# Kernel optimization log

Hardware: AMD Instinct MI355X
Metric: run time of the kernel (lower is better)

Reference implementation:

```python
import jax, jax.numpy as jnp
import numpy as np

D = 1024        # model dim (== moe_inter_dim, required by Expert's x2*x3)
H = 1024        # expert hidden dim (moe_inter_dim)
E = 8           # n_routed_experts
K = 2           # n_activated_experts (top-k)
I = 2 * 1024    # shared-expert inter dim = n_shared_experts * moe_inter_dim
ROUTE_SCALE = 1.0


def setup_inputs() -> dict:
    key = jax.random.key(0)
    ks = jax.random.split(key, 12)
    s = lambda *sh: 1.0 / np.sqrt(sh[-1])
    return {
        "x":      jax.random.normal(ks[0], (1, 2048, D), jnp.float32),
        "gate_w": jax.random.normal(ks[1], (E, D), jnp.float32) * s(E, D),
        "w1":     jax.random.normal(ks[2], (E, H, D), jnp.float32) * s(H, D),
        "b1":     jax.random.normal(ks[3], (E, H), jnp.float32) * 0.01,
        "w2":     jax.random.normal(ks[4], (E, D, H), jnp.float32) * s(D, H),
        "b2":     jax.random.normal(ks[5], (E, D), jnp.float32) * 0.01,
        "w3":     jax.random.normal(ks[6], (E, H, D), jnp.float32) * s(H, D),
        "b3":     jax.random.normal(ks[7], (E, H), jnp.float32) * 0.01,
        "sw1":    jax.random.normal(ks[8], (I, D), jnp.float32) * s(I, D),
        "sw2":    jax.random.normal(ks[9], (I, D), jnp.float32) * s(I, D),
        "sw3":    jax.random.normal(ks[10], (D, I), jnp.float32) * s(D, I),
    }


def reference(x, gate_w, w1, b1, w2, b2, w3, b3, sw1, sw2, sw3):
    B, S, _ = x.shape
    xt = x.reshape(-1, D)                                  # (T, D)
    # ---- Gate (softmax scoring, n_groups==1, no bias, route_scale=1) ----
    logits = xt @ gate_w.T                                 # (T, E)
    scores = jax.nn.softmax(logits.astype(jnp.float32), axis=-1)
    top_vals, idx = jax.lax.top_k(scores, K)               # (T, K)
    weights = (jnp.take_along_axis(scores, idx, axis=1)
               .astype(x.dtype)) * ROUTE_SCALE             # (T, K)
    # ---- Routed experts: input is scaled by routing weight BEFORE expert ----
    xs = xt[:, None, :] * weights[:, :, None]              # (T, K, D)
    y = jnp.zeros_like(xt)
    for e in range(E):  # fixed small loop over experts (dense masked dispatch)
        mask = (idx == e).astype(x.dtype)                  # (T, K)
        h = jax.nn.silu(jnp.einsum('tkd,hd->tkh', xs, w1[e]) + b1[e])
        x2 = jnp.einsum('tkh,dh->tkd', h, w2[e]) + b2[e]   # (T, K, D)
        x3 = jnp.einsum('tkd,hd->tkh', xs, w3[e]) + b3[e]  # (T, K, H==D)
        y = y + jnp.sum((x2 * x3) * mask[:, :, None], axis=1)
    # ---- Shared experts (SwiGLU MLP, no biases) ----
    z = (jax.nn.silu(xt @ sw1.T) * (xt @ sw2.T)) @ sw3.T   # (T, D)
    return (y + z).reshape(B, S, D)
```

## Files before the change

kernel.cpp:

```cpp
#include <hip/hip_runtime.h>

typedef unsigned short u16;
typedef __attribute__((ext_vector_type(4))) float floatx4;
typedef __attribute__((ext_vector_type(8))) short short8;

#define MAXROWS 5120

__device__ __forceinline__ u16 f2bf(float f) {
    union { float f; unsigned u; } v; v.f = f;
    unsigned r = v.u + 0x7FFF + ((v.u >> 16) & 1);
    return (u16)(r >> 16);
}
__device__ __forceinline__ float bf2f(u16 h) {
    union { unsigned u; float f; } v; v.u = ((unsigned)h) << 16; return v.f;
}
__device__ __forceinline__ float silu_f(float x) { return x / (1.f + __expf(-x)); }

__device__ __forceinline__ void gl_lds16(const void* g, void* l) {
    __builtin_amdgcn_global_load_lds(
        (__attribute__((address_space(1))) unsigned int*)g,
        (__attribute__((address_space(3))) unsigned int*)l, 16, 0, 0);
}

__device__ __forceinline__ void ld_frags(
    unsigned a0, unsigned a1, unsigned a2, unsigned a3,
    unsigned b0, unsigned b1, unsigned b2, unsigned b3,
    short8& af0, short8& af1, short8& af2, short8& af3,
    short8& bf0, short8& bf1, short8& bf2, short8& bf3) {
    asm volatile(
        "ds_read_b128 %0, %8\n\t"
        "ds_read_b128 %1, %9\n\t"
        "ds_read_b128 %2, %10\n\t"
        "ds_read_b128 %3, %11\n\t"
        "ds_read_b128 %4, %12\n\t"
        "ds_read_b128 %5, %13\n\t"
        "ds_read_b128 %6, %14\n\t"
        "ds_read_b128 %7, %15\n\t"
        "s_waitcnt lgkmcnt(0)"
        : "=&v"(af0), "=&v"(af1), "=&v"(af2), "=&v"(af3),
          "=&v"(bf0), "=&v"(bf1), "=&v"(bf2), "=&v"(bf3)
        : "v"(a0), "v"(a1), "v"(a2), "v"(a3),
          "v"(b0), "v"(b1), "v"(b2), "v"(b3));
}

#define WAIT_VM6() __builtin_amdgcn_s_waitcnt(3958)
#define WAIT_VM3() __builtin_amdgcn_s_waitcnt(3955)
#define WAIT_VM0() __builtin_amdgcn_s_waitcnt(3952)
#define BAR()      __builtin_amdgcn_s_barrier()

__global__ void conv_gate(const float* __restrict__ w1, const float* __restrict__ w2,
                          const float* __restrict__ w3, const float* __restrict__ sw1,
                          const float* __restrict__ sw2, const float* __restrict__ sw3,
                          const float* __restrict__ x, const float* __restrict__ gw,
                          u16* __restrict__ W13, u16* __restrict__ W2b,
                          u16* __restrict__ S12, u16* __restrict__ S3b,
                          u16* __restrict__ Xb,
                          int* __restrict__ idxA, float* __restrict__ wA) {
    int bid = blockIdx.x;
    if (bid < 512) {
        int w = threadIdx.x >> 6, lane = threadIdx.x & 63;
        int t = bid * 4 + w;
        const float* xr = x + (size_t)t * 1024;
        float acc[8];
#pragma unroll
        for (int e = 0; e < 8; e++) acc[e] = 0.f;
#pragma unroll
        for (int i = 0; i < 16; i++) {
            float xv = xr[lane + (i << 6)];
#pragma unroll
            for (int e = 0; e < 8; e++) acc[e] += xv * gw[e * 1024 + lane + (i << 6)];
        }
#pragma unroll
        for (int e = 0; e < 8; e++)
            for (int off = 32; off > 0; off >>= 1) acc[e] += __shfl_xor(acc[e], off);
        if (lane == 0) {
            float m = acc[0];
#pragma unroll
            for (int e = 1; e < 8; e++) m = fmaxf(m, acc[e]);
            float p[8], s = 0.f;
#pragma unroll
            for (int e = 0; e < 8; e++) { p[e] = __expf(acc[e] - m); s += p[e]; }
            float inv = 1.f / s;
#pragma unroll
            for (int e = 0; e < 8; e++) p[e] *= inv;
            int i0 = 0;
#pragma unroll
            for (int e = 1; e < 8; e++) if (p[e] > p[i0]) i0 = e;
            int i1 = (i0 == 0) ? 1 : 0;
            for (int e = i1 + 1; e < 8; e++) if (e != i0 && p[e] > p[i1]) i1 = e;
            idxA[2 * t] = i0; idxA[2 * t + 1] = i1;
            wA[2 * t] = p[i0]; wA[2 * t + 1] = p[i1];
        }
        return;
    }
    long j = (long)(bid - 512) * 256 + threadIdx.x;
    const float* src; u16* dst; long d;
    if (j < 2097152) {
        long e = j >> 18; src = w1; dst = W13; d = j + (e << 18);
    } else if ((j -= 2097152) < 2097152) {
        long e = j >> 18; src = w3; dst = W13; d = j + (e << 18) + 262144;
    } else if ((j -= 2097152) < 2097152) { src = w2;  dst = W2b; d = j; }
    else if ((j -= 2097152) < 524288) {
        long rr = j >> 8, c4 = j & 255;
        long br = ((rr >> 4) << 5) + (rr & 15);
        src = sw1; dst = S12; d = (br << 8) + c4;
    } else if ((j -= 524288) < 524288) {
        long rr = j >> 8, c4 = j & 255;
        long br = ((rr >> 4) << 5) + 16 + (rr & 15);
        src = sw2; dst = S12; d = (br << 8) + c4;
    } else if ((j -= 524288) < 524288)     { src = sw3; dst = S3b; d = j; }
    else { j -= 524288; src = x; dst = Xb; d = j; }
    float4 v = ((const float4*)src)[j];
    ushort4 o; o.x = f2bf(v.x); o.y = f2bf(v.y); o.z = f2bf(v.z); o.w = f2bf(v.w);
    ((ushort4*)dst)[d] = o;
}

__global__ void rank_k(const int* __restrict__ idxA, int* __restrict__ tileexp,
                       int* __restrict__ tilem0, int* __restrict__ tilevalid,
                       int* __restrict__ ntiles, int* __restrict__ slot_of) {
    int lane = threadIdx.x;
    const int4* my4 = (const int4*)(idxA + lane * 64);
    int h[8];
#pragma unroll
    for (int e = 0; e < 8; e++) h[e] = 0;
    for (int k = 0; k < 16; k++) {
        int4 t = my4[k];
#pragma unroll
        for (int e = 0; e < 8; e++)
            h[e] += (t.x == e) + (t.y == e) + (t.z == e) + (t.w == e);
    }
    int excl[8], tot[8];
#pragma unroll
    for (int e = 0; e < 8; e++) {
        int inc = h[e];
        for (int off = 1; off < 64; off <<= 1) {
            int up = __shfl_up(inc, off);
            if (lane >= off) inc += up;
        }
        excl[e] = inc - h[e];
        tot[e] = __shfl(inc, 63);
    }
    int base[8], tiles = 0;
#pragma unroll
    for (int e = 0; e < 8; e++) {
        base[e] = tiles * 128;
        tiles += (tot[e] + 127) >> 7;
    }
    if (lane == 0) {
        int t256 = 0;
        for (int e = 0; e < 8; e++) {
            int t128 = (tot[e] + 127) >> 7;
            for (int j = 0; j < t128; j += 2) {
                tileexp[t256] = e;
                tilem0[t256] = base[e] + (j << 7);
                tilevalid[t256] = ((t128 - j) >= 2) ? 256 : 128;
                t256++;
            }
        }
        ntiles[0] = t256;
    }
    int c[8];
#pragma unroll
    for (int e = 0; e < 8; e++) c[e] = base[e] + excl[e];
    int4* so4 = (int4*)(slot_of + lane * 64);
    for (int k = 0; k < 16; k++) {
        int4 t = my4[k];
        int4 s;
        int sx = 0;
#pragma unroll
        for (int e = 0; e < 8; e++) sx += (t.x == e) ? c[e] : 0;
#pragma unroll
        for (int e = 0; e < 8; e++) c[e] += (t.x == e);
        int sy = 0;
#pragma unroll
        for (int e = 0; e < 8; e++) sy += (t.y == e) ? c[e] : 0;
#pragma unroll
        for (int e = 0; e < 8; e++) c[e] += (t.y == e);
        int sz = 0;
#pragma unroll
        for (int e = 0; e < 8; e++) sz += (t.z == e) ? c[e] : 0;
#pragma unroll
        for (int e = 0; e < 8; e++) c[e] += (t.z == e);
        int sw = 0;
#pragma unroll
        for (int e = 0; e < 8; e++) sw += (t.w == e) ? c[e] : 0;
#pragma unroll
        for (int e = 0; e < 8; e++) c[e] += (t.w == e);
        s.x = sx; s.y = sy; s.z = sz; s.w = sw;
        so4[k] = s;
    }
}

__global__ void build_xs(const float* __restrict__ x, const float* __restrict__ wA,
                         const int* __restrict__ slot_of, u16* __restrict__ XS) {
    int s = blockIdx.x, i = threadIdx.x;
    int t = s >> 1; float w = wA[s]; int slot = slot_of[s];
    float4 v = ((const float4*)(x + (size_t)t * 1024))[i];
    ushort4 o; o.x = f2bf(v.x * w); o.y = f2bf(v.y * w); o.z = f2bf(v.z * w); o.w = f2bf(v.w * w);
    ((ushort4*)(XS + (size_t)slot * 1024))[i] = o;
}

#define STAGE3(BUF, Ab, Bb, lda, kk)                                           \
    {                                                                          \
        int rA_ = (w << 4) + rloc;                                             \
        int cgA_ = clds ^ ((rA_ >> 1) & 3);                                    \
        gl_lds16((Ab) + (size_t)(m0 + rA_) * (lda) + (kk) + (cgA_ << 3),       \
                 LDS + (BUF) * 12288 + (w << 9));                              \
        int rA2_ = rA_ + 128;                                                  \
        int cgA2_ = clds ^ ((rA2_ >> 1) & 3);                                  \
        gl_lds16((Ab) + (size_t)(m0 + rA2_) * (lda) + (kk) + (cgA2_ << 3),     \
                 LDS + (BUF) * 12288 + (w << 9) + 4096);                       \
        gl_lds16((Bb) + (size_t)(n0 + rA_) * (lda) + (kk) + (cgA_ << 3),       \
                 LDS + (BUF) * 12288 + 8192 + (w << 9));                       \
    }

#define COMPUTE(BUF)                                                           \
    {                                                                          \
        unsigned bo = (unsigned)(BUF) * 24576u;                                \
        short8 af[4], bf[4];                                                   \
        ld_frags(adA[0] + bo, adA[1] + bo, adA[2] + bo, adA[3] + bo,           \
                 adB[0] + bo, adB[1] + bo, adB[2] + bo, adB[3] + bo,           \
                 af[0], af[1], af[2], af[3], bf[0], bf[1], bf[2], bf[3]);      \
        __builtin_amdgcn_s_setprio(1);                                         \
        _Pragma("unroll")                                                      \
        for (int i_ = 0; i_ < 4; i_++)                                         \
            _Pragma("unroll")                                                  \
            for (int j_ = 0; j_ < 4; j_++)                                     \
                acc[i_][j_] = __builtin_amdgcn_mfma_f32_16x16x32_bf16(         \
                    af[i_], bf[j_], acc[i_][j_], 0, 0, 0);                     \
        __builtin_amdgcn_s_setprio(0);                                         \
    }

#define KLOOP(NSTEP, Ab, Bb, lda, kbeg)                                        \
    {                                                                          \
        STAGE3(0, Ab, Bb, lda, (kbeg));                                        \
        STAGE3(1, Ab, Bb, lda, (kbeg) + 32);                                   \
        for (int t = 0; t < (NSTEP); t++) {                                    \
            if (t + 2 < (NSTEP)) {                                             \
                STAGE3((t + 2) % 3, Ab, Bb, lda, (kbeg) + ((t + 2) << 5));     \
                WAIT_VM6();                                                    \
            } else if (t + 1 < (NSTEP)) {                                      \
                WAIT_VM3();                                                    \
            } else {                                                           \
                WAIT_VM0();                                                    \
            }                                                                  \
            BAR();                                                             \
            COMPUTE(t % 3);                                                    \
            BAR();                                                             \
        }                                                                      \
    }

#define GEMM_PRE()                                                             \
    int tid = threadIdx.x, w = tid >> 6, lane = tid & 63;                      \
    int wm = w >> 1, wn = w & 1;                                               \
    int rloc = lane >> 2, clds = lane & 3, q = lane >> 4, l15 = lane & 15;     \
    unsigned ldsbase = (unsigned)(size_t)(__attribute__((address_space(3))) u16*)LDS; \
    unsigned adA[4], adB[4];                                                   \
    _Pragma("unroll")                                                          \
    for (int i = 0; i < 4; i++) {                                              \
        int rr = (wm << 6) + (i << 4) + l15;                                   \
        int g = q ^ ((rr >> 1) & 3);                                           \
        adA[i] = ldsbase + rr * 64 + g * 16;                                   \
    }                                                                          \
    _Pragma("unroll")                                                          \
    for (int j = 0; j < 4; j++) {                                              \
        int rr = (wn << 6) + (j << 4) + l15;                                   \
        int g = q ^ ((rr >> 1) & 3);                                           \
        adB[j] = ldsbase + 16384 + rr * 64 + g * 16;                           \
    }                                                                          \
    floatx4 acc[4][4];                                                         \
    _Pragma("unroll")                                                          \
    for (int i = 0; i < 4; i++)                                                \
        _Pragma("unroll")                                                      \
        for (int j = 0; j < 4; j++) {                                          \
            floatx4 z = {0.f, 0.f, 0.f, 0.f}; acc[i][j] = z;                   \
        }

__global__ __launch_bounds__(512, 4) void gemm_A(
    const u16* __restrict__ XS, const u16* __restrict__ Xb,
    const u16* __restrict__ W13, const u16* __restrict__ S12,
    const float* __restrict__ b1, const float* __restrict__ b3,
    u16* __restrict__ H, u16* __restrict__ X3h, u16* __restrict__ G,
    const int* __restrict__ tileexp, const int* __restrict__ tilem0,
    const int* __restrict__ tilevalid, const int* __restrict__ ntiles) {
    __shared__ u16 LDS[36864];
    int bid = blockIdx.x;
    const u16 *Ab, *Bb; int m0, n0, nt = 0, e = 0, vcnt = 256; bool routed;
    if (bid < 640) {
        routed = true;
        int mt = bid >> 4;
        nt = bid & 15;
        if (mt >= ntiles[0]) return;
        e = tileexp[mt]; m0 = tilem0[mt]; vcnt = tilevalid[mt];
        n0 = nt << 7;
        Ab = XS; Bb = W13 + ((size_t)e << 21);
    } else {
        routed = false; int s = bid - 640;
        m0 = (s >> 5) << 8; n0 = (s & 31) << 7;
        Ab = Xb; Bb = S12;
    }
    GEMM_PRE();

    KLOOP(32, Ab, Bb, 1024, 0);

    if (routed) {
#pragma unroll
        for (int i = 0; i < 4; i++) {
            if (((wm << 6) + (i << 4)) >= vcnt) continue;
            int rowb = m0 + (wm << 6) + (i << 4) + (q << 2);
#pragma unroll
            for (int j = 0; j < 4; j++) {
                int col = n0 + (wn << 6) + (j << 4) + l15;
#pragma unroll
                for (int r = 0; r < 4; r++) {
                    float v = acc[i][j][r];
                    int rw = rowb + r;
                    if (nt < 8) {
                        H[(size_t)rw * 1024 + col] = f2bf(silu_f(v + b1[e * 1024 + col]));
                    } else {
                        int c2 = col - 1024;
                        X3h[(size_t)rw * 1024 + c2] = f2bf(v + b3[e * 1024 + c2]);
                    }
                }
            }
        }
    } else {
#pragma unroll
        for (int i = 0; i < 4; i++) {
            int rowb = m0 + (wm << 6) + (i << 4) + (q << 2);
#pragma unroll
            for (int jp = 0; jp < 4; jp += 2) {
                int brb = n0 + (wn << 6) + (jp << 4);
                int lcol = ((brb >> 5) << 4) + l15;
#pragma unroll
                for (int r = 0; r < 4; r++) {
                    float u = acc[i][jp][r], v = acc[i][jp + 1][r];
                    G[(size_t)(rowb + r) * 2048 + lcol] = f2bf(silu_f(u) * v);
                }
            }
        }
    }
}

__global__ __launch_bounds__(512, 4) void gemm_B(
    const u16* __restrict__ H, const u16* __restrict__ G,
    const u16* __restrict__ W2b, const u16* __restrict__ S3b,
    const float* __restrict__ b2, const u16* __restrict__ X3h,
    u16* __restrict__ P0, u16* __restrict__ P1, float* __restrict__ Z,
    const int* __restrict__ tileexp, const int* __restrict__ tilem0,
    const int* __restrict__ tilevalid, const int* __restrict__ ntiles) {
    __shared__ u16 LDS[36864];
    int bid = blockIdx.x;
    const u16 *Ab, *Bb; int m0, n0, kc, kbeg, lda, np, e = 0, vcnt = 256; bool routed;
    if (bid < 640) {
        routed = true;
        int mt = bid >> 4;
        int r = bid & 15; int nt = r & 7; kc = r >> 3;
        if (mt >= ntiles[0]) return;
        e = tileexp[mt]; m0 = tilem0[mt]; vcnt = tilevalid[mt];
        n0 = nt << 7;
        Ab = H; Bb = W2b + ((size_t)e << 20); lda = 1024; kbeg = kc << 9; np = 16;
    } else {
        routed = false; int s = bid - 640;
        m0 = (s >> 4) << 8; n0 = ((s & 15) >> 1) << 7; kc = s & 1;
        Ab = G; Bb = S3b; lda = 2048; kbeg = kc << 10; np = 32;
    }
    GEMM_PRE();

    KLOOP(np, Ab, Bb, lda, kbeg);

    if (routed) {
        u16* Pk = kc ? P1 : P0;
#pragma unroll
        for (int i = 0; i < 4; i++) {
            if (((wm << 6) + (i << 4)) >= vcnt) continue;
            int rowb = m0 + (wm << 6) + (i << 4) + (q << 2);
#pragma unroll
            for (int j = 0; j < 4; j++) {
                int col = n0 + (wn << 6) + (j << 4) + l15;
#pragma unroll
                for (int r = 0; r < 4; r++) {
                    int rw = rowb + r;
                    float v = acc[i][j][r] + (kc == 0 ? b2[e * 1024 + col] : 0.f);
                    float pv = v * bf2f(X3h[(size_t)rw * 1024 + col]);
                    Pk[(size_t)rw * 1024 + col] = f2bf(pv);
                }
            }
        }
    } else {
        float* Zk = Z + (size_t)kc * 2097152;
#pragma unroll
        for (int i = 0; i < 4; i++) {
            int rowb = m0 + (wm << 6) + (i << 4) + (q << 2);
#pragma unroll
            for (int j = 0; j < 4; j++) {
                int col = n0 + (wn << 6) + (j << 4) + l15;
#pragma unroll
                for (int r = 0; r < 4; r++)
                    Zk[(size_t)(rowb + r) * 1024 + col] = acc[i][j][r];
            }
        }
    }
}

__global__ void final_k(const float* __restrict__ Z,
                        const u16* __restrict__ P0, const u16* __restrict__ P1,
                        const int* __restrict__ slot_of, float* __restrict__ out) {
    int i = blockIdx.x * 256 + threadIdx.x;
    int t = i >> 8, c4 = i & 255;
    int s0 = slot_of[2 * t], s1 = slot_of[2 * t + 1];
    size_t zi = (size_t)t * 256 + c4;
    float4 z0 = ((const float4*)Z)[zi];
    float4 z1 = ((const float4*)(Z + 2097152))[zi];
    ushort4 a0 = ((const ushort4*)P0)[(size_t)s0 * 256 + c4];
    ushort4 a1 = ((const ushort4*)P1)[(size_t)s0 * 256 + c4];
    ushort4 c0 = ((const ushort4*)P0)[(size_t)s1 * 256 + c4];
    ushort4 c1 = ((const ushort4*)P1)[(size_t)s1 * 256 + c4];
    float4 o;
    o.x = z0.x + z1.x + bf2f(a0.x) + bf2f(a1.x) + bf2f(c0.x) + bf2f(c1.x);
    o.y = z0.y + z1.y + bf2f(a0.y) + bf2f(a1.y) + bf2f(c0.y) + bf2f(c1.y);
    o.z = z0.z + z1.z + bf2f(a0.z) + bf2f(a1.z) + bf2f(c0.z) + bf2f(c1.z);
    o.w = z0.w + z1.w + bf2f(a0.w) + bf2f(a1.w) + bf2f(c0.w) + bf2f(c1.w);
    ((float4*)out)[(size_t)t * 256 + c4] = o;
}

extern "C" void kernel_launch(void* const* d_in, const int* in_sizes, int n_in,
                              void* d_out, int out_size, void* d_ws, size_t ws_size,
                              hipStream_t stream) {
    const float* x   = (const float*)d_in[0];
    const float* gw  = (const float*)d_in[1];
    const float* w1  = (const float*)d_in[2];
    const float* b1  = (const float*)d_in[3];
    const float* w2  = (const float*)d_in[4];
    const float* b2  = (const float*)d_in[5];
    const float* w3  = (const float*)d_in[6];
    const float* b3  = (const float*)d_in[7];
    const float* sw1 = (const float*)d_in[8];
    const float* sw2 = (const float*)d_in[9];
    const float* sw3 = (const float*)d_in[10];
    float* out = (float*)d_out;

    char* p = (char*)d_ws;
    int* ntiles    = (int*)(p + 192);
    int* tileexp   = (int*)(p + 256);
    int* tilem0    = (int*)(p + 512);
    int* tilevalid = (int*)(p + 768);
    size_t off = 4096;
    u16*   XS      = (u16*)(p + off);   off += (size_t)MAXROWS * 1024 * 2;
    int*   idxA    = (int*)(p + off);   off += 16384;
    float* wA      = (float*)(p + off); off += 16384;
    int*   slot_of = (int*)(p + off);   off += 16384;
    u16*   H       = (u16*)(p + off);   off += (size_t)MAXROWS * 1024 * 2;
    u16*   X3h     = (u16*)(p + off);   off += (size_t)MAXROWS * 1024 * 2;
    u16*   P0      = (u16*)(p + off);   off += (size_t)MAXROWS * 1024 * 2;
    u16*   P1      = (u16*)(p + off);   off += (size_t)MAXROWS * 1024 * 2;
    float* Z       = (float*)(p + off); off += (size_t)4 * 2048 * 1024 * 4;
    u16*   W13     = (u16*)(p + off);   off += (size_t)8 * 2048 * 1024 * 2;
    u16*   W2b     = (u16*)(p + off);   off += (size_t)8 * 1024 * 1024 * 2;
    u16*   S12     = (u16*)(p + off);   off += (size_t)4096 * 1024 * 2;
    u16*   S3b     = (u16*)(p + off);   off += (size_t)1024 * 2048 * 2;
    u16*   Xb      = (u16*)(p + off);   off += (size_t)2048 * 1024 * 2;
    u16*   G       = (u16*)(p + off);   off += (size_t)2048 * 2048 * 2;

    conv_gate<<<33280, 256, 0, stream>>>(w1, w2, w3, sw1, sw2, sw3, x, gw,
                                         W13, W2b, S12, S3b, Xb, idxA, wA);
    rank_k<<<1, 64, 0, stream>>>(idxA, tileexp, tilem0, tilevalid, ntiles, slot_of);
    build_xs<<<4096, 256, 0, stream>>>(x, wA, slot_of, XS);

    gemm_A<<<896, 512, 0, stream>>>(XS, Xb, W13, S12, b1, b3, H, X3h, G,
                                    tileexp, tilem0, tilevalid, ntiles);
    gemm_B<<<768, 512, 0, stream>>>(H, G, W2b, S3b, b2, X3h, P0, P1, Z,
                                    tileexp, tilem0, tilevalid, ntiles);
    final_k<<<2048, 256, 0, stream>>>(Z, P0, P1, slot_of, out);
}
```

Measured before the change: 290.7 us.

## Switch GEMMs to 128x128 tiles with persistent balanced work distribution

Replaces the fixed 256x128 tiles (512 threads) with 128x128 tiles (256 threads) and launches a fixed grid of 768 blocks. Each block loops over a contiguous, evenly divided range of work units, so the routed blocks that previously exited early no longer leave the grid unbalanced. The shared-expert down projection now splits K four ways, and the final kernel sums four partial Z buffers instead of two. Smaller tiles mean less data reuse per block and more partial-sum traffic to global memory, in exchange for finer load balance and no padded 256-row tiles.

```diff
diff --git a/kernel.cpp b/kernel.cpp
--- a/kernel.cpp
+++ b/kernel.cpp
@@ -5,6 +5,7 @@
 typedef __attribute__((ext_vector_type(8))) short short8;
 
 #define MAXROWS 5120
+#define NB 768
 
 __device__ __forceinline__ u16 f2bf(float f) {
     union { float f; unsigned u; } v; v.f = f;
@@ -43,8 +44,8 @@
           "v"(b0), "v"(b1), "v"(b2), "v"(b3));
 }
 
-#define WAIT_VM6() __builtin_amdgcn_s_waitcnt(3958)
-#define WAIT_VM3() __builtin_amdgcn_s_waitcnt(3955)
+#define WAIT_VM8() __builtin_amdgcn_s_waitcnt(3960)
+#define WAIT_VM4() __builtin_amdgcn_s_waitcnt(3956)
 #define WAIT_VM0() __builtin_amdgcn_s_waitcnt(3952)
 #define BAR()      __builtin_amdgcn_s_barrier()
 
@@ -116,7 +117,6 @@
 }
 
 __global__ void rank_k(const int* __restrict__ idxA, int* __restrict__ tileexp,
-                       int* __restrict__ tilem0, int* __restrict__ tilevalid,
                        int* __restrict__ ntiles, int* __restrict__ slot_of) {
     int lane = threadIdx.x;
     const int4* my4 = (const int4*)(idxA + lane * 64);
@@ -147,17 +147,12 @@
         tiles += (tot[e] + 127) >> 7;
     }
     if (lane == 0) {
-        int t256 = 0;
+        int t = 0;
         for (int e = 0; e < 8; e++) {
-            int t128 = (tot[e] + 127) >> 7;
-            for (int j = 0; j < t128; j += 2) {
-                tileexp[t256] = e;
-                tilem0[t256] = base[e] + (j << 7);
-                tilevalid[t256] = ((t128 - j) >= 2) ? 256 : 128;
-                t256++;
-            }
-        }
-        ntiles[0] = t256;
+            int te = (tot[e] + 127) >> 7;
+            for (int j = 0; j < te; j++) tileexp[t++] = e;
+        }
+        ntiles[0] = t;
     }
     int c[8];
 #pragma unroll
@@ -200,23 +195,23 @@
     ((ushort4*)(XS + (size_t)slot * 1024))[i] = o;
 }
 
-#define STAGE3(BUF, Ab, Bb, lda, kk)                                           \
+#define STAGE(BUF, Ab, Bb, lda, kk)                                            \
     {                                                                          \
-        int rA_ = (w << 4) + rloc;                                             \
-        int cgA_ = clds ^ ((rA_ >> 1) & 3);                                    \
-        gl_lds16((Ab) + (size_t)(m0 + rA_) * (lda) + (kk) + (cgA_ << 3),       \
-                 LDS + (BUF) * 12288 + (w << 9));                              \
-        int rA2_ = rA_ + 128;                                                  \
-        int cgA2_ = clds ^ ((rA2_ >> 1) & 3);                                  \
-        gl_lds16((Ab) + (size_t)(m0 + rA2_) * (lda) + (kk) + (cgA2_ << 3),     \
-                 LDS + (BUF) * 12288 + (w << 9) + 4096);                       \
-        gl_lds16((Bb) + (size_t)(n0 + rA_) * (lda) + (kk) + (cgA_ << 3),       \
-                 LDS + (BUF) * 12288 + 8192 + (w << 9));                       \
+        _Pragma("unroll")                                                      \
+        for (int t2 = 0; t2 < 2; t2++) {                                       \
+            int r_ = (w << 4) + (t2 << 6) + rloc;                              \
+            int cg_ = clds ^ ((r_ >> 1) & 3);                                  \
+            int db_ = (BUF) * 8192 + ((w << 4) + (t2 << 6)) * 32;              \
+            gl_lds16((Ab) + (size_t)(m0 + r_) * (lda) + (kk) + (cg_ << 3),     \
+                     LDS + db_);                                               \
+            gl_lds16((Bb) + (size_t)(n0 + r_) * (lda) + (kk) + (cg_ << 3),     \
+                     LDS + 4096 + db_);                                        \
+        }                                                                      \
     }
 
 #define COMPUTE(BUF)                                                           \
     {                                                                          \
-        unsigned bo = (unsigned)(BUF) * 24576u;                                \
+        unsigned bo = (unsigned)(BUF) * 16384u;                                \
         short8 af[4], bf[4];                                                   \
         ld_frags(adA[0] + bo, adA[1] + bo, adA[2] + bo, adA[3] + bo,           \
                  adB[0] + bo, adB[1] + bo, adB[2] + bo, adB[3] + bo,           \
@@ -231,16 +226,16 @@
         __builtin_amdgcn_s_setprio(0);                                         \
     }
 
-#define KLOOP(NSTEP, Ab, Bb, lda, kbeg)                                        \
+#define KLOOP(NP, Ab, Bb, lda, kbeg)                                           \
     {                                                                          \
-        STAGE3(0, Ab, Bb, lda, (kbeg));                                        \
-        STAGE3(1, Ab, Bb, lda, (kbeg) + 32);                                   \
-        for (int t = 0; t < (NSTEP); t++) {                                    \
-            if (t + 2 < (NSTEP)) {                                             \
-                STAGE3((t + 2) % 3, Ab, Bb, lda, (kbeg) + ((t + 2) << 5));     \
-                WAIT_VM6();                                                    \
-            } else if (t + 1 < (NSTEP)) {                                      \
-                WAIT_VM3();                                                    \
+        STAGE(0, Ab, Bb, lda, (kbeg));                                         \
+        STAGE(1, Ab, Bb, lda, (kbeg) + 32);                                    \
+        for (int t = 0; t < (NP); t++) {                                       \
+            if (t + 2 < (NP)) {                                                \
+                STAGE((t + 2) % 3, Ab, Bb, lda, (kbeg) + ((t + 2) << 5));      \
+                WAIT_VM8();                                                    \
+            } else if (t + 1 < (NP)) {                                         \
+                WAIT_VM4();                                                    \
             } else {                                                           \
                 WAIT_VM0();                                                    \
             }                                                                  \
@@ -266,8 +261,10 @@
     for (int j = 0; j < 4; j++) {                                              \
         int rr = (wn << 6) + (j << 4) + l15;                                   \
         int g = q ^ ((rr >> 1) & 3);                                           \
-        adB[j] = ldsbase + 16384 + rr * 64 + g * 16;                           \
-    }                                                                          \
+        adB[j] = ldsbase + 8192 + rr * 64 + g * 16;                            \
+    }
+
+#define ACC_ZERO()                                                             \
     floatx4 acc[4][4];                                                         \
     _Pragma("unroll")                                                          \
     for (int i = 0; i < 4; i++)                                                \
@@ -276,128 +273,128 @@
             floatx4 z = {0.f, 0.f, 0.f, 0.f}; acc[i][j] = z;                   \
         }
 
-__global__ __launch_bounds__(512, 4) void gemm_A(
+__global__ __launch_bounds__(256, 3) void gemm_A(
     const u16* __restrict__ XS, const u16* __restrict__ Xb,
     const u16* __restrict__ W13, const u16* __restrict__ S12,
     const float* __restrict__ b1, const float* __restrict__ b3,
     u16* __restrict__ H, u16* __restrict__ X3h, u16* __restrict__ G,
-    const int* __restrict__ tileexp, const int* __restrict__ tilem0,
-    const int* __restrict__ tilevalid, const int* __restrict__ ntiles) {
-    __shared__ u16 LDS[36864];
+    const int* __restrict__ tileexp, const int* __restrict__ ntiles) {
+    __shared__ u16 LDS[24576];
+    GEMM_PRE();
+    int n128 = ntiles[0];
+    int routedU = n128 << 4;
+    int NU = routedU + 512;
     int bid = blockIdx.x;
-    const u16 *Ab, *Bb; int m0, n0, nt = 0, e = 0, vcnt = 256; bool routed;
-    if (bid < 640) {
-        routed = true;
-        int mt = bid >> 4;
-        nt = bid & 15;
-        if (mt >= ntiles[0]) return;
-        e = tileexp[mt]; m0 = tilem0[mt]; vcnt = tilevalid[mt];
-        n0 = nt << 7;
-        Ab = XS; Bb = W13 + ((size_t)e << 21);
-    } else {
-        routed = false; int s = bid - 640;
-        m0 = (s >> 5) << 8; n0 = (s & 31) << 7;
-        Ab = Xb; Bb = S12;
-    }
-    GEMM_PRE();
-
-    KLOOP(32, Ab, Bb, 1024, 0);
-
-    if (routed) {
-#pragma unroll
-        for (int i = 0; i < 4; i++) {
-            if (((wm << 6) + (i << 4)) >= vcnt) continue;
-            int rowb = m0 + (wm << 6) + (i << 4) + (q << 2);
-#pragma unroll
-            for (int j = 0; j < 4; j++) {
-                int col = n0 + (wn << 6) + (j << 4) + l15;
-#pragma unroll
-                for (int r = 0; r < 4; r++) {
-                    float v = acc[i][j][r];
-                    int rw = rowb + r;
-                    if (nt < 8) {
-                        H[(size_t)rw * 1024 + col] = f2bf(silu_f(v + b1[e * 1024 + col]));
-                    } else {
-                        int c2 = col - 1024;
-                        X3h[(size_t)rw * 1024 + c2] = f2bf(v + b3[e * 1024 + c2]);
+    int u0 = (bid * NU) / NB, u1 = ((bid + 1) * NU) / NB;
+    for (int u = u0; u < u1; u++) {
+        const u16 *Ab, *Bb; int m0, n0, nt = 0, e = 0; bool routed;
+        if (u < routedU) {
+            routed = true;
+            int mt = u >> 4; nt = u & 15;
+            e = tileexp[mt]; m0 = mt << 7; n0 = nt << 7;
+            Ab = XS; Bb = W13 + ((size_t)e << 21);
+        } else {
+            routed = false; int s = u - routedU;
+            m0 = (s >> 5) << 7; n0 = (s & 31) << 7;
+            Ab = Xb; Bb = S12;
+        }
+        ACC_ZERO();
+        KLOOP(32, Ab, Bb, 1024, 0);
+        if (routed) {
+#pragma unroll
+            for (int i = 0; i < 4; i++) {
+                int rowb = m0 + (wm << 6) + (i << 4) + (q << 2);
+#pragma unroll
+                for (int j = 0; j < 4; j++) {
+                    int col = n0 + (wn << 6) + (j << 4) + l15;
+#pragma unroll
+                    for (int r = 0; r < 4; r++) {
+                        float v = acc[i][j][r];
+                        int rw = rowb + r;
+                        if (nt < 8) {
+                            H[(size_t)rw * 1024 + col] = f2bf(silu_f(v + b1[e * 1024 + col]));
+                        } else {
+                            int c2 = col - 1024;
+                            X3h[(size_t)rw * 1024 + c2] = f2bf(v + b3[e * 1024 + c2]);
+                        }
                     }
                 }
             }
-        }
-    } else {
-#pragma unroll
-        for (int i = 0; i < 4; i++) {
-            int rowb = m0 + (wm << 6) + (i << 4) + (q << 2);
-#pragma unroll
-            for (int jp = 0; jp < 4; jp += 2) {
-                int brb = n0 + (wn << 6) + (jp << 4);
-                int lcol = ((brb >> 5) << 4) + l15;
-#pragma unroll
-                for (int r = 0; r < 4; r++) {
-                    float u = acc[i][jp][r], v = acc[i][jp + 1][r];
-                    G[(size_t)(rowb + r) * 2048 + lcol] = f2bf(silu_f(u) * v);
+        } else {
+#pragma unroll
+            for (int i = 0; i < 4; i++) {
+                int rowb = m0 + (wm << 6) + (i << 4) + (q << 2);
+#pragma unroll
+                for (int jp = 0; jp < 4; jp += 2) {
+                    int brb = n0 + (wn << 6) + (jp << 4);
+                    int lcol = ((brb >> 5) << 4) + l15;
+#pragma unroll
+                    for (int r = 0; r < 4; r++) {
+                        float uu = acc[i][jp][r], v = acc[i][jp + 1][r];
+                        G[(size_t)(rowb + r) * 2048 + lcol] = f2bf(silu_f(uu) * v);
+                    }
                 }
             }
         }
     }
 }
 
-__global__ __launch_bounds__(512, 4) void gemm_B(
+__global__ __launch_bounds__(256, 3) void gemm_B(
     const u16* __restrict__ H, const u16* __restrict__ G,
     const u16* __restrict__ W2b, const u16* __restrict__ S3b,
     const float* __restrict__ b2, const u16* __restrict__ X3h,
     u16* __restrict__ P0, u16* __restrict__ P1, float* __restrict__ Z,
-    const int* __restrict__ tileexp, const int* __restrict__ tilem0,
-    const int* __restrict__ tilevalid, const int* __restrict__ ntiles) {
-    __shared__ u16 LDS[36864];
+    const int* __restrict__ tileexp, const int* __restrict__ ntiles) {
+    __shared__ u16 LDS[24576];
+    GEMM_PRE();
+    int n128 = ntiles[0];
+    int routedU = n128 << 4;
+    int NU = routedU + 512;
     int bid = blockIdx.x;
-    const u16 *Ab, *Bb; int m0, n0, kc, kbeg, lda, np, e = 0, vcnt = 256; bool routed;
-    if (bid < 640) {
-        routed = true;
-        int mt = bid >> 4;
-        int r = bid & 15; int nt = r & 7; kc = r >> 3;
-        if (mt >= ntiles[0]) return;
-        e = tileexp[mt]; m0 = tilem0[mt]; vcnt = tilevalid[mt];
-        n0 = nt << 7;
-        Ab = H; Bb = W2b + ((size_t)e << 20); lda = 1024; kbeg = kc << 9; np = 16;
-    } else {
-        routed = false; int s = bid - 640;
-        m0 = (s >> 4) << 8; n0 = ((s & 15) >> 1) << 7; kc = s & 1;
-        Ab = G; Bb = S3b; lda = 2048; kbeg = kc << 10; np = 32;
-    }
-    GEMM_PRE();
-
-    KLOOP(np, Ab, Bb, lda, kbeg);
-
-    if (routed) {
-        u16* Pk = kc ? P1 : P0;
-#pragma unroll
-        for (int i = 0; i < 4; i++) {
-            if (((wm << 6) + (i << 4)) >= vcnt) continue;
-            int rowb = m0 + (wm << 6) + (i << 4) + (q << 2);
-#pragma unroll
-            for (int j = 0; j < 4; j++) {
-                int col = n0 + (wn << 6) + (j << 4) + l15;
-#pragma unroll
-                for (int r = 0; r < 4; r++) {
-                    int rw = rowb + r;
-                    float v = acc[i][j][r] + (kc == 0 ? b2[e * 1024 + col] : 0.f);
-                    float pv = v * bf2f(X3h[(size_t)rw * 1024 + col]);
-                    Pk[(size_t)rw * 1024 + col] = f2bf(pv);
+    int u0 = (bid * NU) / NB, u1 = ((bid + 1) * NU) / NB;
+    for (int u = u0; u < u1; u++) {
+        const u16 *Ab, *Bb; int m0, n0, kc, kbeg, lda, e = 0; bool routed;
+        if (u < routedU) {
+            routed = true;
+            int mt = u >> 4; int r = u & 15; int nt = r & 7; kc = r >> 3;
+            e = tileexp[mt]; m0 = mt << 7; n0 = nt << 7;
+            Ab = H; Bb = W2b + ((size_t)e << 20); lda = 1024; kbeg = kc << 9;
+        } else {
+            routed = false; int s = u - routedU;
+            m0 = (s >> 5) << 7; int r = s & 31; n0 = (r >> 2) << 7; kc = r & 3;
+            Ab = G; Bb = S3b; lda = 2048; kbeg = kc << 9;
+        }
+        ACC_ZERO();
+        KLOOP(16, Ab, Bb, lda, kbeg);
+        if (routed) {
+            u16* Pk = kc ? P1 : P0;
+#pragma unroll
+            for (int i = 0; i < 4; i++) {
+                int rowb = m0 + (wm << 6) + (i << 4) + (q << 2);
+#pragma unroll
+                for (int j = 0; j < 4; j++) {
+                    int col = n0 + (wn << 6) + (j << 4) + l15;
+#pragma unroll
+                    for (int r = 0; r < 4; r++) {
+                        int rw = rowb + r;
+                        float v = acc[i][j][r] + (kc == 0 ? b2[e * 1024 + col] : 0.f);
+                        float pv = v * bf2f(X3h[(size_t)rw * 1024 + col]);
+                        Pk[(size_t)rw * 1024 + col] = f2bf(pv);
+                    }
                 }
             }
-        }
-    } else {
-        float* Zk = Z + (size_t)kc * 2097152;
-#pragma unroll
-        for (int i = 0; i < 4; i++) {
-            int rowb = m0 + (wm << 6) + (i << 4) + (q << 2);
-#pragma unroll
-            for (int j = 0; j < 4; j++) {
-                int col = n0 + (wn << 6) + (j << 4) + l15;
-#pragma unroll
-                for (int r = 0; r < 4; r++)
-                    Zk[(size_t)(rowb + r) * 1024 + col] = acc[i][j][r];
+        } else {
+            float* Zk = Z + (size_t)kc * 2097152;
+#pragma unroll
+            for (int i = 0; i < 4; i++) {
+                int rowb = m0 + (wm << 6) + (i << 4) + (q << 2);
+#pragma unroll
+                for (int j = 0; j < 4; j++) {
+                    int col = n0 + (wn << 6) + (j << 4) + l15;
+#pragma unroll
+                    for (int r = 0; r < 4; r++)
+                        Zk[(size_t)(rowb + r) * 1024 + col] = acc[i][j][r];
+                }
             }
         }
     }
@@ -412,15 +409,17 @@
     size_t zi = (size_t)t * 256 + c4;
     float4 z0 = ((const float4*)Z)[zi];
     float4 z1 = ((const float4*)(Z + 2097152))[zi];
+    float4 z2 = ((const float4*)(Z + 4194304))[zi];
+    float4 z3 = ((const float4*)(Z + 6291456))[zi];
     ushort4 a0 = ((const ushort4*)P0)[(size_t)s0 * 256 + c4];
     ushort4 a1 = ((const ushort4*)P1)[(size_t)s0 * 256 + c4];
     ushort4 c0 = ((const ushort4*)P0)[(size_t)s1 * 256 + c4];
     ushort4 c1 = ((const ushort4*)P1)[(size_t)s1 * 256 + c4];
     float4 o;
-    o.x = z0.x + z1.x + bf2f(a0.x) + bf2f(a1.x) + bf2f(c0.x) + bf2f(c1.x);
-    o.y = z0.y + z1.y + bf2f(a0.y) + bf2f(a1.y) + bf2f(c0.y) + bf2f(c1.y);
-    o.z = z0.z + z1.z + bf2f(a0.z) + bf2f(a1.z) + bf2f(c0.z) + bf2f(c1.z);
-    o.w = z0.w + z1.w + bf2f(a0.w) + bf2f(a1.w) + bf2f(c0.w) + bf2f(c1.w);
+    o.x = z0.x + z1.x + z2.x + z3.x + bf2f(a0.x) + bf2f(a1.x) + bf2f(c0.x) + bf2f(c1.x);
+    o.y = z0.y + z1.y + z2.y + z3.y + bf2f(a0.y) + bf2f(a1.y) + bf2f(c0.y) + bf2f(c1.y);
+    o.z = z0.z + z1.z + z2.z + z3.z + bf2f(a0.z) + bf2f(a1.z) + bf2f(c0.z) + bf2f(c1.z);
+    o.w = z0.w + z1.w + z2.w + z3.w + bf2f(a0.w) + bf2f(a1.w) + bf2f(c0.w) + bf2f(c1.w);
     ((float4*)out)[(size_t)t * 256 + c4] = o;
 }
 
@@ -441,10 +440,8 @@
     float* out = (float*)d_out;
 
     char* p = (char*)d_ws;
-    int* ntiles    = (int*)(p + 192);
-    int* tileexp   = (int*)(p + 256);
-    int* tilem0    = (int*)(p + 512);
-    int* tilevalid = (int*)(p + 768);
+    int* ntiles  = (int*)(p + 192);
+    int* tileexp = (int*)(p + 256);
     size_t off = 4096;
     u16*   XS      = (u16*)(p + off);   off += (size_t)MAXROWS * 1024 * 2;
     int*   idxA    = (int*)(p + off);   off += 16384;
@@ -464,12 +461,12 @@
 
     conv_gate<<<33280, 256, 0, stream>>>(w1, w2, w3, sw1, sw2, sw3, x, gw,
                                          W13, W2b, S12, S3b, Xb, idxA, wA);
-    rank_k<<<1, 64, 0, stream>>>(idxA, tileexp, tilem0, tilevalid, ntiles, slot_of);
+    rank_k<<<1, 64, 0, stream>>>(idxA, tileexp, ntiles, slot_of);
     build_xs<<<4096, 256, 0, stream>>>(x, wA, slot_of, XS);
 
-    gemm_A<<<896, 512, 0, stream>>>(XS, Xb, W13, S12, b1, b3, H, X3h, G,
-                                    tileexp, tilem0, tilevalid, ntiles);
-    gemm_B<<<768, 512, 0, stream>>>(H, G, W2b, S3b, b2, X3h, P0, P1, Z,
-                                    tileexp, tilem0, tilevalid, ntiles);
+    gemm_A<<<NB, 256, 0, stream>>>(XS, Xb, W13, S12, b1, b3, H, X3h, G,
+                                   tileexp, ntiles);
+    gemm_B<<<NB, 256, 0, stream>>>(H, G, W2b, S3b, b2, X3h, P0, P1, Z,
+                                   tileexp, ntiles);
     final_k<<<2048, 256, 0, stream>>>(Z, P0, P1, slot_of, out);
 }
```

After: 357.7 us. +23.1%, slower.
